# Performance work log

Measured on AMD Instinct MI355X. Metric: run time of the kernel, lower is better.

Reference implementation:

```python
import jax, jax.numpy as jnp
import numpy as np

B, S, HID = 2, 4096, 2048
NH, NKV, HD = 16, 4, 128  # num_heads, num_kv_heads, head_dim
GROUPS = NH // NKV
ROPE_THETA = 10000.0


def _rope_cos_sin(position_ids):
    # position_ids: [B, S] int
    inv_freq = 1.0 / (ROPE_THETA ** (jnp.arange(0, HD, 2, dtype=jnp.float32) / HD))  # [HD/2]
    freqs = position_ids.astype(jnp.float32)[..., None] * inv_freq  # [B, S, HD/2]
    emb = jnp.concatenate([freqs, freqs], axis=-1)  # [B, S, HD]
    return jnp.cos(emb), jnp.sin(emb)


def _rotate_half(x):
    x1, x2 = jnp.split(x, 2, axis=-1)
    return jnp.concatenate([-x2, x1], axis=-1)


def _apply_rope(q, k, cos, sin):
    # q: [B, NH, S, HD], k: [B, NKV, S, HD]; cos/sin: [B, S, HD]
    cos = cos[:, None, :, :]
    sin = sin[:, None, :, :]
    q = q * cos + _rotate_half(q) * sin
    k = k * cos + _rotate_half(k) * sin
    return q, k


def kappa(x):
    return jax.nn.elu(x) + 1.0


def setup_inputs() -> dict:
    key = jax.random.key(0)
    ks = jax.random.split(key, 8)
    sc = 0.02
    hidden_states = jax.random.normal(ks[0], (B, S, HID), dtype=jnp.float32)
    position_ids = jnp.broadcast_to(jnp.arange(S, dtype=jnp.int64)[None, :], (B, S))
    Wq = jax.random.normal(ks[1], (HID, NH * HD), dtype=jnp.float32) * sc
    Wk = jax.random.normal(ks[2], (HID, NKV * HD), dtype=jnp.float32) * sc
    Wv = jax.random.normal(ks[3], (HID, NKV * HD), dtype=jnp.float32) * sc
    Wo = jax.random.normal(ks[4], (HID, HID), dtype=jnp.float32) * sc
    Wphi = jax.random.normal(ks[5], (HID, HID), dtype=jnp.float32) * sc
    bphi = jax.random.normal(ks[6], (HID,), dtype=jnp.float32) * sc
    return {"hidden_states": hidden_states, "position_ids": position_ids,
            "Wq": Wq, "Wk": Wk, "Wv": Wv, "Wo": Wo, "Wphi": Wphi, "bphi": bphi}


def reference(hidden_states, position_ids, Wq, Wk, Wv, Wo, Wphi, bphi):
    b, s, _ = hidden_states.shape
    # projections -> [B, heads, S, HD]
    q = (hidden_states @ Wq).reshape(b, s, NH, HD).transpose(0, 2, 1, 3)
    k = (hidden_states @ Wk).reshape(b, s, NKV, HD).transpose(0, 2, 1, 3)
    v = (hidden_states @ Wv).reshape(b, s, NKV, HD).transpose(0, 2, 1, 3)
    cos, sin = _rope_cos_sin(position_ids)
    q, k = _apply_rope(q, k, cos, sin)
    # GQA expand kv heads
    k = jnp.repeat(k, GROUPS, axis=1)  # [B, NH, S, HD]
    v = jnp.repeat(v, GROUPS, axis=1)
    Qk = kappa(q)
    Kk = kappa(k)
    Qg = Qk.mean(axis=2)  # [B, NH, HD]
    logits = jnp.einsum('bnd,bnsd->bns', Qg, Kk)
    alpha = jax.nn.softmax(logits, axis=-1) * float(s)  # [B, NH, S]
    outer_sum = jnp.einsum('bns,bnsd,bnsf->bndf', alpha, Kk, v)  # [B, NH, HD, HD]
    X_phi = (hidden_states @ Wphi + bphi).reshape(b, s, NH, HD).transpose(0, 2, 1, 3)
    result_attn = jnp.einsum('bnsd,bndf->bnsf', Qk, outer_sum)
    context = (X_phi * result_attn).transpose(0, 2, 1, 3).reshape(b, s, HID)
    return context @ Wo
```

## Files before the change

kernel.cpp:

```cpp
#include <hip/hip_runtime.h>
#include <hip/hip_bf16.h>
#include <math.h>

#define B_    2
#define S_    4096
#define HID_  2048
#define NH_   16
#define NKV_  4
#define HD_   128
#define GROUPS_ (NH_/NKV_)
#define ROPE_THETA_ 10000.0f
#define OSPLIT 8
#define QCH   32

typedef __attribute__((ext_vector_type(8))) short short8;
typedef __attribute__((ext_vector_type(4))) float f32x4;

__device__ inline unsigned short f2bf(float f) {
    __hip_bfloat16 h = __float2bfloat16(f);
    return *(unsigned short*)&h;
}

__device__ inline void gload16(const void* g, void* l) {
    __builtin_amdgcn_global_load_lds((const __attribute__((address_space(1))) void*)g,
                                     (__attribute__((address_space(3))) void*)l, 16, 0, 0);
}

#define BARM() asm volatile("s_barrier" ::: "memory")

__global__ void rope_table_kernel(float* __restrict__ cosT, float* __restrict__ sinT) {
    int s = blockIdx.x;
    int i = threadIdx.x;
    float expo = -2.0f * (float)i / (float)HD_;
    float invf = powf(ROPE_THETA_, expo);
    float f = (float)s * invf;
    cosT[s * 64 + i] = cosf(f);
    sinT[s * 64 + i] = sinf(f);
}

__global__ void cast_bf16_kernel(const float* __restrict__ in,
                                 __hip_bfloat16* __restrict__ out, int n8) {
    int i = blockIdx.x * 256 + threadIdx.x;
    if (i >= n8) return;
    const float4 v0 = *reinterpret_cast<const float4*>(&in[i * 8]);
    const float4 v1 = *reinterpret_cast<const float4*>(&in[i * 8 + 4]);
    union { short8 v; unsigned short u[8]; } o;
    o.u[0] = f2bf(v0.x); o.u[1] = f2bf(v0.y); o.u[2] = f2bf(v0.z); o.u[3] = f2bf(v0.w);
    o.u[4] = f2bf(v1.x); o.u[5] = f2bf(v1.y); o.u[6] = f2bf(v1.z); o.u[7] = f2bf(v1.w);
    *reinterpret_cast<short8*>(&out[i * 8]) = o.v;
}

__global__ __launch_bounds__(256) void transpose_cast_kernel(
        const float* __restrict__ W, __hip_bfloat16* __restrict__ Wt, int K, int N) {
    __shared__ float T[64][65];
    int k0 = blockIdx.y * 64, n0 = blockIdx.x * 64;
    int tid = threadIdx.x;
    int r = tid >> 4, c4 = (tid & 15) * 4;
#pragma unroll
    for (int p = 0; p < 4; ++p) {
        float4 v = *reinterpret_cast<const float4*>(&W[(size_t)(k0 + r + p * 16) * N + n0 + c4]);
        T[r + p * 16][c4 + 0] = v.x;
        T[r + p * 16][c4 + 1] = v.y;
        T[r + p * 16][c4 + 2] = v.z;
        T[r + p * 16][c4 + 3] = v.w;
    }
    __syncthreads();
#pragma unroll
    for (int p = 0; p < 4; ++p) {
        int n = r + p * 16;
        short4 o;
        o.x = (short)f2bf(T[c4 + 0][n]);
        o.y = (short)f2bf(T[c4 + 1][n]);
        o.z = (short)f2bf(T[c4 + 2][n]);
        o.w = (short)f2bf(T[c4 + 3][n]);
        *reinterpret_cast<short4*>(&Wt[(size_t)(n0 + n) * K + k0 + c4]) = o;
    }
}

#define BM 128
#define BN 128
#define BKK 32
__global__ __launch_bounds__(256) void gemm_mfma_kernel(
        const __hip_bfloat16* __restrict__ A, const __hip_bfloat16* __restrict__ Bt,
        float* __restrict__ C, const float* __restrict__ bias, int M, int N, int K) {
    __shared__ __hip_bfloat16 As[BM * BKK];
    __shared__ __hip_bfloat16 Bs[BN * BKK];
    int tid  = threadIdx.x;
    int wid  = tid >> 6, lane = tid & 63;
    int wr   = wid >> 1, wc = wid & 1;
    int bm = blockIdx.y * BM, bn = blockIdx.x * BN;

    f32x4 acc[4][4];
#pragma unroll
    for (int m = 0; m < 4; ++m)
#pragma unroll
        for (int n = 0; n < 4; ++n)
#pragma unroll
            for (int i = 0; i < 4; ++i) acc[m][n][i] = 0.0f;

    int srow = tid >> 2;
    int scol = (tid & 3) * 8;
    const __hip_bfloat16* aS0 = A  + (size_t)(bm + srow)      * K + scol;
    const __hip_bfloat16* aS1 = A  + (size_t)(bm + 64 + srow) * K + scol;
    const __hip_bfloat16* bS0 = Bt + (size_t)(bn + srow)      * K + scol;
    const __hip_bfloat16* bS1 = Bt + (size_t)(bn + 64 + srow) * K + scol;
    __hip_bfloat16* aD0 = &As[wid * 512];
    __hip_bfloat16* aD1 = &As[2048 + wid * 512];
    __hip_bfloat16* bD0 = &Bs[wid * 512];
    __hip_bfloat16* bD1 = &Bs[2048 + wid * 512];

    int lr = lane & 15;
    int kq = (lane >> 4) * 8;

    for (int k0 = 0; k0 < K; k0 += BKK) {
        gload16(aS0 + k0, aD0);
        gload16(aS1 + k0, aD1);
        gload16(bS0 + k0, bD0);
        gload16(bS1 + k0, bD1);
        __syncthreads();

        short8 af[4], bf[4];
#pragma unroll
        for (int m = 0; m < 4; ++m)
            af[m] = *reinterpret_cast<short8*>(&As[(wr * 64 + m * 16 + lr) * BKK + kq]);
#pragma unroll
        for (int n = 0; n < 4; ++n)
            bf[n] = *reinterpret_cast<short8*>(&Bs[(wc * 64 + n * 16 + lr) * BKK + kq]);
#pragma unroll
        for (int m = 0; m < 4; ++m)
#pragma unroll
            for (int n = 0; n < 4; ++n)
                acc[m][n] = __builtin_amdgcn_mfma_f32_16x16x32_bf16(
                    af[m], bf[n], acc[m][n], 0, 0, 0);
        __syncthreads();
    }

    int lq = lane >> 4;
#pragma unroll
    for (int m = 0; m < 4; ++m) {
#pragma unroll
        for (int n = 0; n < 4; ++n) {
            int row = bm + wr * 64 + m * 16 + lq * 4;
            int col = bn + wc * 64 + n * 16 + lr;
            float bv = (bias != nullptr) ? bias[col] : 0.0f;
#pragma unroll
            for (int r = 0; r < 4; ++r)
                C[(size_t)(row + r) * N + col] = acc[m][n][r] + bv;
        }
    }
}

#define TBUFEL 16384

__device__ __forceinline__ void stage_region(const __hip_bfloat16* __restrict__ src,
        int ldK, int row0, int kbase, __hip_bfloat16* dst, int tid) {
#pragma unroll
    for (int g = 0; g < 2; ++g) {
        int P = g * 512 + tid;
        int row = P >> 2, cp = P & 3;
        int cl = cp ^ ((row >> 1) & 3);
        gload16(src + (size_t)(row0 + row) * ldK + kbase + cl * 8, dst + P * 8);
    }
}

__global__ __launch_bounds__(512, 2) void gemm_mfma256_kernel(
        const __hip_bfloat16* __restrict__ A, const __hip_bfloat16* __restrict__ Bt,
        float* __restrict__ C, __hip_bfloat16* __restrict__ Cb,
        const float* __restrict__ bias, int M, int N, int K) {
    __shared__ __hip_bfloat16 lds[4 * TBUFEL];
    int tid = threadIdx.x, lane = tid & 63, wid = tid >> 6;
    int wr = wid >> 2, wc = wid & 3;
    int lr = lane & 15, lc = lane >> 4;
    int c16 = lc ^ ((lr >> 1) & 3);

    int nwg = gridDim.x;
    int orig = blockIdx.x;
    int q = nwg >> 3, r = nwg & 7;
    int xcd = orig & 7, lid = orig >> 3;
    int wg = (xcd < r ? xcd * (q + 1) : r * (q + 1) + (xcd - r) * q) + lid;
    int tiles_n = N >> 8;
    int bm = (wg / tiles_n) << 8, bn = (wg % tiles_n) << 8;

    f32x4 acc[8][4];
#pragma unroll
    for (int m = 0; m < 8; ++m)
#pragma unroll
        for (int n = 0; n < 4; ++n)
#pragma unroll
            for (int i = 0; i < 4; ++i) acc[m][n][i] = 0.0f;

    const int NKT = K >> 5;

    stage_region(A,  K, bm, 0,  lds,                 tid);
    stage_region(Bt, K, bn, 0,  lds + 8192,          tid);
    stage_region(A,  K, bm, 32, lds + TBUFEL,        tid);
    stage_region(Bt, K, bn, 32, lds + TBUFEL + 8192, tid);
    asm volatile("s_waitcnt vmcnt(4)" ::: "memory");
    BARM();

    for (int kt = 0; kt < NKT; ++kt) {
        __hip_bfloat16* buf = lds + (size_t)(kt & 3) * TBUFEL;
        __hip_bfloat16* stg = lds + (size_t)((kt + 2) & 3) * TBUFEL;
        const bool pf = (kt + 2 < NKT);

        if (pf) stage_region(A, K, bm, (kt + 2) << 5, stg, tid);
        short8 a0[4], b0[4];
#pragma unroll
        for (int m = 0; m < 4; ++m)
            a0[m] = *reinterpret_cast<const short8*>(
                &buf[(size_t)(wr * 128 + m * 16 + lr) * 32 + c16 * 8]);
#pragma unroll
        for (int n = 0; n < 4; ++n)
            b0[n] = *reinterpret_cast<const short8*>(
                &buf[8192 + (size_t)(wc * 64 + n * 16 + lr) * 32 + c16 * 8]);
        BARM();
        __builtin_amdgcn_s_setprio(1);
#pragma unroll
        for (int m = 0; m < 4; ++m)
#pragma unroll
            for (int n = 0; n < 4; ++n)
                acc[m][n] = __builtin_amdgcn_mfma_f32_16x16x32_bf16(
                    a0[m], b0[n], acc[m][n], 0, 0, 0);
        __builtin_amdgcn_s_setprio(0);
        BARM();

        if (pf) stage_region(Bt, K, bn, (kt + 2) << 5, stg + 8192, tid);
        short8 a1[4];
#pragma unroll
        for (int m = 0; m < 4; ++m)
            a1[m] = *reinterpret_cast<const short8*>(
                &buf[(size_t)(wr * 128 + 64 + m * 16 + lr) * 32 + c16 * 8]);
        BARM();
        __builtin_amdgcn_s_setprio(1);
#pragma unroll
        for (int m = 0; m < 4; ++m)
#pragma unroll
            for (int n = 0; n < 4; ++n)
                acc[m + 4][n] = __builtin_amdgcn_mfma_f32_16x16x32_bf16(
                    a1[m], b0[n], acc[m + 4][n], 0, 0, 0);
        __builtin_amdgcn_s_setprio(0);
        if (pf) { asm volatile("s_waitcnt vmcnt(4)" ::: "memory"); }
        else    { asm volatile("s_waitcnt vmcnt(0)" ::: "memory"); }
        BARM();
    }

    int lq = lane >> 4;
#pragma unroll
    for (int m = 0; m < 8; ++m) {
#pragma unroll
        for (int n = 0; n < 4; ++n) {
            int row = bm + wr * 128 + m * 16 + lq * 4;
            int col = bn + wc * 64 + n * 16 + lr;
            float bv = (bias != nullptr) ? bias[col] : 0.0f;
            if (Cb != nullptr) {
#pragma unroll
                for (int rr = 0; rr < 4; ++rr)
                    Cb[(size_t)(row + rr) * N + col] = __float2bfloat16(acc[m][n][rr] + bv);
            } else {
#pragma unroll
                for (int rr = 0; rr < 4; ++rr)
                    C[(size_t)(row + rr) * N + col] = acc[m][n][rr] + bv;
            }
        }
    }
}

__global__ void rope_kappa_kernel(float* __restrict__ X,
                                  const float* __restrict__ cosT,
                                  const float* __restrict__ sinT,
                                  int nheads, int rs, int total) {
    int idx = blockIdx.x * blockDim.x + threadIdx.x;
    if (idx >= total) return;
    int d  = idx & 63;
    int t  = idx >> 6;
    int n  = t % nheads;
    int bs = t / nheads;
    int s  = bs % S_;
    size_t base = (size_t)bs * rs + n * HD_;
    float c = cosT[s * 64 + d];
    float sn = sinT[s * 64 + d];
    float x1 = X[base + d];
    float x2 = X[base + d + 64];
    float r1 = x1 * c - x2 * sn;
    float r2 = x2 * c + x1 * sn;
    r1 = (r1 > 0.0f) ? (r1 + 1.0f) : expf(r1);
    r2 = (r2 > 0.0f) ? (r2 + 1.0f) : expf(r2);
    X[base + d] = r1;
    X[base + d + 64] = r2;
}

__global__ __launch_bounds__(128) void qg_partial_kernel(
        const float* __restrict__ Qk, float* __restrict__ QPART) {
    int blk = blockIdx.x;
    int c   = blk % QCH;
    int bn  = blk / QCH;
    int b = bn / NH_, n = bn % NH_;
    int d = threadIdx.x;
    float acc = 0.0f;
    int s0 = c * (S_ / QCH);
    for (int s = s0; s < s0 + S_ / QCH; ++s)
        acc += Qk[((size_t)b * S_ + s) * (NH_ * HD_) + n * HD_ + d];
    QPART[(size_t)(c * (B_ * NH_) + bn) * HD_ + d] = acc;
}

__global__ __launch_bounds__(256) void qg_reduce_kernel(
        const float* __restrict__ QPART, float* __restrict__ QG) {
    int idx = blockIdx.x * 256 + threadIdx.x;
    float acc = 0.0f;
#pragma unroll
    for (int c = 0; c < QCH; ++c)
        acc += QPART[(size_t)c * (B_ * NH_ * HD_) + idx];
    QG[idx] = acc * (1.0f / (float)S_);
}

__global__ __launch_bounds__(256) void logits_kernel(
        const float* __restrict__ KV, const float* __restrict__ QG,
        float* __restrict__ LG) {
    int bk = blockIdx.x;
    int b = bk / NKV_, kn = bk % NKV_;
    int s0 = blockIdx.y * 256;
    int w = threadIdx.x >> 6, lane = threadIdx.x & 63;
    float2 qv[GROUPS_];
#pragma unroll
    for (int g = 0; g < GROUPS_; ++g)
        qv[g] = *reinterpret_cast<const float2*>(
            &QG[(size_t)(b * NH_ + kn * GROUPS_ + g) * HD_ + lane * 2]);
    for (int i = 0; i < 64; ++i) {
        int s = s0 + w * 64 + i;
        float2 kv = *reinterpret_cast<const float2*>(
            &KV[((size_t)b * S_ + s) * 1024 + kn * HD_ + lane * 2]);
        float p[GROUPS_];
#pragma unroll
        for (int g = 0; g < GROUPS_; ++g) p[g] = kv.x * qv[g].x + kv.y * qv[g].y;
#pragma unroll
        for (int off = 32; off > 0; off >>= 1)
#pragma unroll
            for (int g = 0; g < GROUPS_; ++g) p[g] += __shfl_xor(p[g], off);
        if (lane == 0) {
#pragma unroll
            for (int g = 0; g < GROUPS_; ++g)
                LG[(size_t)(b * NH_ + kn * GROUPS_ + g) * S_ + s] = p[g];
        }
    }
}

__global__ __launch_bounds__(256) void softmax_alpha_kernel(float* __restrict__ LG) {
    int bn = blockIdx.x;
    float* row = &LG[(size_t)bn * S_];
    __shared__ float lg[S_];
    __shared__ float red[256];
    int tid = threadIdx.x;
    float lmax = -1e30f;
    for (int s = tid; s < S_; s += 256) {
        float v = row[s];
        lg[s] = v;
        lmax = fmaxf(lmax, v);
    }
    red[tid] = lmax;
    __syncthreads();
    for (int off = 128; off > 0; off >>= 1) {
        if (tid < off) red[tid] = fmaxf(red[tid], red[tid + off]);
        __syncthreads();
    }
    float mx = red[0];
    __syncthreads();
    float lsum = 0.0f;
    for (int s = tid; s < S_; s += 256) {
        float e = expf(lg[s] - mx);
        lg[s] = e;
        lsum += e;
    }
    red[tid] = lsum;
    __syncthreads();
    for (int off = 128; off > 0; off >>= 1) {
        if (tid < off) red[tid] += red[tid + off];
        __syncthreads();
    }
    float inv = (float)S_ / red[0];
    for (int s = tid; s < S_; s += 256)
        row[s] = lg[s] * inv;
}

__global__ __launch_bounds__(256) void kvt_kernel(
        const float* __restrict__ KV, const float* __restrict__ ALPHA,
        __hip_bfloat16* __restrict__ AKT, __hip_bfloat16* __restrict__ VT) {
    int bk = blockIdx.x;
    int b = bk / NKV_, kn = bk % NKV_;
    int s0 = blockIdx.y * 64;
    int isV = blockIdx.z;
    __shared__ float T[64][HD_ + 4];
    __shared__ float alf[GROUPS_][64];
    int tid = threadIdx.x;

    int r = tid >> 2;
    int c0 = (tid & 3) * 32;
    const float* src = KV + ((size_t)(b * S_) + s0 + r) * 1024 + isV * 512 + kn * HD_ + c0;
#pragma unroll
    for (int i = 0; i < 8; ++i)
        *reinterpret_cast<float4*>(&T[r][c0 + i * 4]) =
            *reinterpret_cast<const float4*>(src + i * 4);
    if (!isV) {
        int g = tid >> 6, ss = tid & 63;
        alf[g][ss] = ALPHA[(size_t)(b * NH_ + kn * GROUPS_ + g) * S_ + s0 + ss];
    }
    __syncthreads();

    int d  = tid >> 1;
    int sh = (tid & 1) * 32;
    if (isV) {
        __hip_bfloat16* dst = VT + ((size_t)bk * HD_ + d) * S_ + s0 + sh;
#pragma unroll
        for (int i = 0; i < 8; ++i) {
            short4 o;
            o.x = (short)f2bf(T[sh + i * 4 + 0][d]);
            o.y = (short)f2bf(T[sh + i * 4 + 1][d]);
            o.z = (short)f2bf(T[sh + i * 4 + 2][d]);
            o.w = (short)f2bf(T[sh + i * 4 + 3][d]);
            *reinterpret_cast<short4*>(dst + i * 4) = o;
        }
    } else {
#pragma unroll
        for (int g = 0; g < GROUPS_; ++g) {
            int n = kn * GROUPS_ + g;
            __hip_bfloat16* dst = AKT + ((size_t)(b * NH_ + n) * HD_ + d) * S_ + s0 + sh;
#pragma unroll
            for (int i = 0; i < 8; ++i) {
                short4 o;
                o.x = (short)f2bf(T[sh + i * 4 + 0][d] * alf[g][sh + i * 4 + 0]);
                o.y = (short)f2bf(T[sh + i * 4 + 1][d] * alf[g][sh + i * 4 + 1]);
                o.z = (short)f2bf(T[sh + i * 4 + 2][d] * alf[g][sh + i * 4 + 2]);
                o.w = (short)f2bf(T[sh + i * 4 + 3][d] * alf[g][sh + i * 4 + 3]);
                *reinterpret_cast<short4*>(dst + i * 4) = o;
            }
        }
    }
}

__global__ __launch_bounds__(256) void outer_mfma_kernel(
        const __hip_bfloat16* __restrict__ AKT, const __hip_bfloat16* __restrict__ VT,
        float* __restrict__ OPT) {
    int bn = blockIdx.x;
    int sp = blockIdx.y;
    int b = bn / NH_, n = bn % NH_;
    int kn = n / GROUPS_;
    const __hip_bfloat16* Abase = AKT + (size_t)bn * HD_ * S_ + sp * (S_ / OSPLIT);
    const __hip_bfloat16* Bbase = VT + (size_t)(b * NKV_ + kn) * HD_ * S_ + sp * (S_ / OSPLIT);
    __shared__ __hip_bfloat16 As[128 * 32];
    __shared__ __hip_bfloat16 Bs[128 * 32];
    int tid = threadIdx.x, lane = tid & 63, wid = tid >> 6;
    int wr = wid >> 1, wc = wid & 1;
    int lr = lane & 15, kq = (lane >> 4) * 8;

    f32x4 acc[4][4];
#pragma unroll
    for (int m = 0; m < 4; ++m)
#pragma unroll
        for (int nn = 0; nn < 4; ++nn)
#pragma unroll
            for (int i = 0; i < 4; ++i) acc[m][nn][i] = 0.0f;

    for (int ks = 0; ks < (S_ / OSPLIT) / 32; ++ks) {
        int k0 = ks * 32;
#pragma unroll
        for (int g = 0; g < 2; ++g) {
            int P = g * 256 + tid;
            int row = P >> 2, gr = P & 3;
            gload16(Abase + (size_t)row * S_ + k0 + gr * 8, As + P * 8);
            gload16(Bbase + (size_t)row * S_ + k0 + gr * 8, Bs + P * 8);
        }
        __syncthreads();
        short8 af[4], bf[4];
#pragma unroll
        for (int m = 0; m < 4; ++m)
            af[m] = *reinterpret_cast<short8*>(&As[(wr * 64 + m * 16 + lr) * 32 + kq]);
#pragma unroll
        for (int nn = 0; nn < 4; ++nn)
            bf[nn] = *reinterpret_cast<short8*>(&Bs[(wc * 64 + nn * 16 + lr) * 32 + kq]);
#pragma unroll
        for (int m = 0; m < 4; ++m)
#pragma unroll
            for (int nn = 0; nn < 4; ++nn)
                acc[m][nn] = __builtin_amdgcn_mfma_f32_16x16x32_bf16(
                    af[m], bf[nn], acc[m][nn], 0, 0, 0);
        __syncthreads();
    }

    float* base = OPT + ((size_t)bn * OSPLIT + sp) * (HD_ * HD_);
    int lq = lane >> 4;
#pragma unroll
    for (int m = 0; m < 4; ++m) {
#pragma unroll
        for (int nn = 0; nn < 4; ++nn) {
            int drow = wr * 64 + m * 16 + lq * 4;
            int fcol = wc * 64 + nn * 16 + lr;
            float4 o;
            o.x = acc[m][nn][0]; o.y = acc[m][nn][1];
            o.z = acc[m][nn][2]; o.w = acc[m][nn][3];
            *reinterpret_cast<float4*>(&base[(size_t)fcol * HD_ + drow]) = o;
        }
    }
}

__global__ __launch_bounds__(256) void outer_reduce_tc_kernel(
        const float* __restrict__ OPT, __hip_bfloat16* __restrict__ OUTt) {
    int idx = blockIdx.x * 256 + threadIdx.x;
    int bn = idx >> 11;
    int rem = idx & 2047;
    int f = rem >> 4, g = rem & 15;
    const float* src = OPT + (size_t)bn * OSPLIT * 16384 + f * 128 + g * 8;
    float s[8] = {};
#pragma unroll
    for (int sp = 0; sp < OSPLIT; ++sp) {
        float4 v0 = *reinterpret_cast<const float4*>(src + (size_t)sp * 16384);
        float4 v1 = *reinterpret_cast<const float4*>(src + (size_t)sp * 16384 + 4);
        s[0] += v0.x; s[1] += v0.y; s[2] += v0.z; s[3] += v0.w;
        s[4] += v1.x; s[5] += v1.y; s[6] += v1.z; s[7] += v1.w;
    }
    int gp = g ^ (f & 7);
    union { short8 v; unsigned short u[8]; } o;
#pragma unroll
    for (int j = 0; j < 8; ++j) o.u[j] = f2bf(s[j]);
    *reinterpret_cast<short8*>(&OUTt[(size_t)bn * 16384 + f * 128 + gp * 8]) = o.v;
}

__global__ __launch_bounds__(256) void attn_context_mfma_kernel(
        const float* __restrict__ Qk, const __hip_bfloat16* __restrict__ OUTt,
        const __hip_bfloat16* __restrict__ XPHIb, __hip_bfloat16* __restrict__ CTX) {
    int bn = blockIdx.x;
    int b = bn / NH_, n = bn % NH_;
    int s0 = blockIdx.y * 256;
    __shared__ __hip_bfloat16 Ms[128 * 128];
    int tid = threadIdx.x, lane = tid & 63, wid = tid >> 6;
    int lr = lane & 15, lc = lane >> 4;

#pragma unroll
    for (int g = 0; g < 8; ++g) {
        int P = g * 256 + tid;
        gload16(OUTt + (size_t)bn * 16384 + (size_t)P * 8, Ms + (size_t)P * 8);
    }

    f32x4 acc[4][8];
#pragma unroll
    for (int m = 0; m < 4; ++m)
#pragma unroll
        for (int nn = 0; nn < 8; ++nn)
#pragma unroll
            for (int i = 0; i < 4; ++i) acc[m][nn][i] = 0.0f;

    __syncthreads();

    const float* qbase = Qk + ((size_t)(b * S_) + s0 + wid * 64) * (NH_ * HD_) + n * HD_;
#pragma unroll
    for (int ks = 0; ks < 4; ++ks) {
        int k8 = ks * 32 + lc * 8;
        short8 a[4];
#pragma unroll
        for (int m = 0; m < 4; ++m) {
            const float* qp = qbase + (size_t)(m * 16 + lr) * (NH_ * HD_) + k8;
            float4 q0 = *reinterpret_cast<const float4*>(qp);
            float4 q1 = *reinterpret_cast<const float4*>(qp + 4);
            union { short8 v; unsigned short u[8]; } cv;
            cv.u[0] = f2bf(q0.x); cv.u[1] = f2bf(q0.y); cv.u[2] = f2bf(q0.z); cv.u[3] = f2bf(q0.w);
            cv.u[4] = f2bf(q1.x); cv.u[5] = f2bf(q1.y); cv.u[6] = f2bf(q1.z); cv.u[7] = f2bf(q1.w);
            a[m] = cv.v;
        }
        int gfull = ks * 4 + lc;
        short8 bb[8];
#pragma unroll
        for (int nn = 0; nn < 8; ++nn) {
            int f = nn * 16 + lr;
            int gp = gfull ^ (f & 7);
            bb[nn] = *reinterpret_cast<const short8*>(&Ms[f * 128 + gp * 8]);
        }
#pragma unroll
        for (int m = 0; m < 4; ++m)
#pragma unroll
            for (int nn = 0; nn < 8; ++nn)
                acc[m][nn] = __builtin_amdgcn_mfma_f32_16x16x32_bf16(
                    a[m], bb[nn], acc[m][nn], 0, 0, 0);
    }

#pragma unroll
    for (int m = 0; m < 4; ++m) {
#pragma unroll
        for (int nn = 0; nn < 8; ++nn) {
            int row = s0 + wid * 64 + m * 16 + lc * 4;
            int f = nn * 16 + lr;
            size_t gi = ((size_t)(b * S_) + row) * (NH_ * HD_) + n * HD_ + f;
#pragma unroll
            for (int r = 0; r < 4; ++r) {
                float xp = __bfloat162float(XPHIb[gi + (size_t)r * (NH_ * HD_)]);
                CTX[gi + (size_t)r * (NH_ * HD_)] = __float2bfloat16(acc[m][nn][r] * xp);
            }
        }
    }
}

extern "C" void kernel_launch(void* const* d_in, const int* in_sizes, int n_in,
                              void* d_out, int out_size, void* d_ws, size_t ws_size,
                              hipStream_t stream) {
    (void)in_sizes; (void)n_in; (void)out_size; (void)ws_size;
    const float* X    = (const float*)d_in[0];
    const float* Wq   = (const float*)d_in[2];
    const float* Wk   = (const float*)d_in[3];
    const float* Wv   = (const float*)d_in[4];
    const float* Wo   = (const float*)d_in[5];
    const float* Wphi = (const float*)d_in[6];
    const float* bphi = (const float*)d_in[7];
    float* out = (float*)d_out;

    float* ws = (float*)d_ws;
    const size_t nQ = (size_t)B_ * S_ * NH_ * HD_;
    const size_t nK = (size_t)B_ * S_ * NKV_ * HD_;
    float* Q     = ws;
    float* KV    = Q + nQ;
    float* XPHI  = KV + 2 * nK;
    float* QG    = XPHI + nQ;
    float* ALPHA = QG + (size_t)B_ * NH_ * HD_;
    float* QPART = ALPHA + (size_t)B_ * NH_ * S_;
    float* COST  = QPART + (size_t)QCH * B_ * NH_ * HD_;
    float* SINT  = COST + (size_t)S_ * 64;
    __hip_bfloat16* Xb    = (__hip_bfloat16*)(SINT + (size_t)S_ * 64);
    __hip_bfloat16* Wqt   = Xb + nQ;
    __hip_bfloat16* Wkt   = Wqt + (size_t)HID_ * (NH_ * HD_);
    __hip_bfloat16* Wvt   = Wkt + (size_t)HID_ * (NKV_ * HD_);
    __hip_bfloat16* Wphit = Wvt + (size_t)HID_ * (NKV_ * HD_);
    __hip_bfloat16* Wot   = Wphit + (size_t)HID_ * (NH_ * HD_);
    __hip_bfloat16* OUTt  = Wot + (size_t)HID_ * HID_;
    __hip_bfloat16* VT    = OUTt + (size_t)B_ * NH_ * HD_ * HD_;
    float* OPT = (float*)(VT + nK);
    __hip_bfloat16* AKT   = Xb;
    __hip_bfloat16* XPHIb = (__hip_bfloat16*)XPHI;
    __hip_bfloat16* CTXb  = (__hip_bfloat16*)KV;

    const int M = B_ * S_;

    rope_table_kernel<<<S_, 64, 0, stream>>>(COST, SINT);
    cast_bf16_kernel<<<(int)(nQ / 8 / 256), 256, 0, stream>>>(X, Xb, (int)(nQ / 8));
    transpose_cast_kernel<<<dim3((NH_ * HD_) / 64, HID_ / 64), 256, 0, stream>>>(Wq, Wqt, HID_, NH_ * HD_);
    transpose_cast_kernel<<<dim3((NKV_ * HD_) / 64, HID_ / 64), 256, 0, stream>>>(Wk, Wkt, HID_, NKV_ * HD_);
    transpose_cast_kernel<<<dim3((NKV_ * HD_) / 64, HID_ / 64), 256, 0, stream>>>(Wv, Wvt, HID_, NKV_ * HD_);
    transpose_cast_kernel<<<dim3((NH_ * HD_) / 64, HID_ / 64), 256, 0, stream>>>(Wphi, Wphit, HID_, NH_ * HD_);
    transpose_cast_kernel<<<dim3(HID_ / 64, HID_ / 64), 256, 0, stream>>>(Wo, Wot, HID_, HID_);

    gemm_mfma256_kernel<<<(M / 256) * ((NH_ * HD_) / 256), 512, 0, stream>>>(
        Xb, Wqt, Q, nullptr, nullptr, M, NH_ * HD_, HID_);
    gemm_mfma_kernel<<<dim3(1024 / BN, M / BM), 256, 0, stream>>>(
        Xb, Wkt, KV, nullptr, M, 1024, HID_);
    gemm_mfma256_kernel<<<(M / 256) * ((NH_ * HD_) / 256), 512, 0, stream>>>(
        Xb, Wphit, nullptr, XPHIb, bphi, M, NH_ * HD_, HID_);

    {
        int totalQ = B_ * S_ * NH_ * 64;
        rope_kappa_kernel<<<totalQ / 256, 256, 0, stream>>>(Q, COST, SINT, NH_, NH_ * HD_, totalQ);
        int totalK = B_ * S_ * NKV_ * 64;
        rope_kappa_kernel<<<totalK / 256, 256, 0, stream>>>(KV, COST, SINT, NKV_, 1024, totalK);
    }

    qg_partial_kernel<<<B_ * NH_ * QCH, 128, 0, stream>>>(Q, QPART);
    qg_reduce_kernel<<<(B_ * NH_ * HD_) / 256, 256, 0, stream>>>(QPART, QG);
    logits_kernel<<<dim3(B_ * NKV_, S_ / 256), 256, 0, stream>>>(KV, QG, ALPHA);
    softmax_alpha_kernel<<<B_ * NH_, 256, 0, stream>>>(ALPHA);

    kvt_kernel<<<dim3(B_ * NKV_, S_ / 64, 2), 256, 0, stream>>>(KV, ALPHA, AKT, VT);
    outer_mfma_kernel<<<dim3(B_ * NH_, OSPLIT), 256, 0, stream>>>(AKT, VT, OPT);
    outer_reduce_tc_kernel<<<(B_ * NH_ * HD_ * 16) / 256, 256, 0, stream>>>(OPT, OUTt);

    attn_context_mfma_kernel<<<dim3(B_ * NH_, S_ / 256), 256, 0, stream>>>(
        Q, OUTt, XPHIb, CTXb);

    gemm_mfma256_kernel<<<(M / 256) * (HID_ / 256), 512, 0, stream>>>(
        CTXb, Wot, out, nullptr, nullptr, M, HID_, HID_);
}
```

Baseline: 473.1 us.

## Store Q in bf16, pipeline the 128-tile GEMM, and trim barriers in the 256 GEMM

The Q projection now writes bf16 output. RoPE+kappa, the Qg partial sums and the context kernel all read and write bf16 Q, which halves Q memory traffic and removes the fp32-to-bf16 conversion in the context kernel. The KV GEMM is rewritten with a 4-buffer swizzled LDS prefetch pipeline using global_load_lds and vmcnt waits. In the 256-tile GEMM, both operand stages are issued up front and the intra-iteration barriers are dropped. The trade-offs are a small precision loss in Q before RoPE/kappa and a possible LDS race if the removed barriers were needed.

```diff
diff --git a/kernel.cpp b/kernel.cpp
--- a/kernel.cpp
+++ b/kernel.cpp
@@ -21,6 +21,12 @@
     return *(unsigned short*)&h;
 }
 
+__device__ inline float bf2f(short u) {
+    union { unsigned int i; float f; } v;
+    v.i = ((unsigned int)(unsigned short)u) << 16;
+    return v.f;
+}
+
 __device__ inline void gload16(const void* g, void* l) {
     __builtin_amdgcn_global_load_lds((const __attribute__((address_space(1))) void*)g,
                                      (__attribute__((address_space(3))) void*)l, 16, 0, 0);
@@ -77,81 +83,6 @@
     }
 }
 
-#define BM 128
-#define BN 128
-#define BKK 32
-__global__ __launch_bounds__(256) void gemm_mfma_kernel(
-        const __hip_bfloat16* __restrict__ A, const __hip_bfloat16* __restrict__ Bt,
-        float* __restrict__ C, const float* __restrict__ bias, int M, int N, int K) {
-    __shared__ __hip_bfloat16 As[BM * BKK];
-    __shared__ __hip_bfloat16 Bs[BN * BKK];
-    int tid  = threadIdx.x;
-    int wid  = tid >> 6, lane = tid & 63;
-    int wr   = wid >> 1, wc = wid & 1;
-    int bm = blockIdx.y * BM, bn = blockIdx.x * BN;
-
-    f32x4 acc[4][4];
-#pragma unroll
-    for (int m = 0; m < 4; ++m)
-#pragma unroll
-        for (int n = 0; n < 4; ++n)
-#pragma unroll
-            for (int i = 0; i < 4; ++i) acc[m][n][i] = 0.0f;
-
-    int srow = tid >> 2;
-    int scol = (tid & 3) * 8;
-    const __hip_bfloat16* aS0 = A  + (size_t)(bm + srow)      * K + scol;
-    const __hip_bfloat16* aS1 = A  + (size_t)(bm + 64 + srow) * K + scol;
-    const __hip_bfloat16* bS0 = Bt + (size_t)(bn + srow)      * K + scol;
-    const __hip_bfloat16* bS1 = Bt + (size_t)(bn + 64 + srow) * K + scol;
-    __hip_bfloat16* aD0 = &As[wid * 512];
-    __hip_bfloat16* aD1 = &As[2048 + wid * 512];
-    __hip_bfloat16* bD0 = &Bs[wid * 512];
-    __hip_bfloat16* bD1 = &Bs[2048 + wid * 512];
-
-    int lr = lane & 15;
-    int kq = (lane >> 4) * 8;
-
-    for (int k0 = 0; k0 < K; k0 += BKK) {
-        gload16(aS0 + k0, aD0);
-        gload16(aS1 + k0, aD1);
-        gload16(bS0 + k0, bD0);
-        gload16(bS1 + k0, bD1);
-        __syncthreads();
-
-        short8 af[4], bf[4];
-#pragma unroll
-        for (int m = 0; m < 4; ++m)
-            af[m] = *reinterpret_cast<short8*>(&As[(wr * 64 + m * 16 + lr) * BKK + kq]);
-#pragma unroll
-        for (int n = 0; n < 4; ++n)
-            bf[n] = *reinterpret_cast<short8*>(&Bs[(wc * 64 + n * 16 + lr) * BKK + kq]);
-#pragma unroll
-        for (int m = 0; m < 4; ++m)
-#pragma unroll
-            for (int n = 0; n < 4; ++n)
-                acc[m][n] = __builtin_amdgcn_mfma_f32_16x16x32_bf16(
-                    af[m], bf[n], acc[m][n], 0, 0, 0);
-        __syncthreads();
-    }
-
-    int lq = lane >> 4;
-#pragma unroll
-    for (int m = 0; m < 4; ++m) {
-#pragma unroll
-        for (int n = 0; n < 4; ++n) {
-            int row = bm + wr * 64 + m * 16 + lq * 4;
-            int col = bn + wc * 64 + n * 16 + lr;
-            float bv = (bias != nullptr) ? bias[col] : 0.0f;
-#pragma unroll
-            for (int r = 0; r < 4; ++r)
-                C[(size_t)(row + r) * N + col] = acc[m][n][r] + bv;
-        }
-    }
-}
-
-#define TBUFEL 16384
-
 __device__ __forceinline__ void stage_region(const __hip_bfloat16* __restrict__ src,
         int ldK, int row0, int kbase, __hip_bfloat16* dst, int tid) {
 #pragma unroll
@@ -162,6 +93,95 @@
         gload16(src + (size_t)(row0 + row) * ldK + kbase + cl * 8, dst + P * 8);
     }
 }
+
+__device__ __forceinline__ void stage_region128(const __hip_bfloat16* __restrict__ src,
+        int ldK, int row0, int kbase, __hip_bfloat16* dst, int tid) {
+#pragma unroll
+    for (int g = 0; g < 2; ++g) {
+        int P = g * 256 + tid;
+        int row = P >> 2, cp = P & 3;
+        int cl = cp ^ ((row >> 1) & 3);
+        gload16(src + (size_t)(row0 + row) * ldK + kbase + cl * 8, dst + P * 8);
+    }
+}
+
+#define BM 128
+#define BN 128
+#define T128EL 8192
+__global__ __launch_bounds__(256) void gemm_mfma_kernel(
+        const __hip_bfloat16* __restrict__ A, const __hip_bfloat16* __restrict__ Bt,
+        float* __restrict__ C, const float* __restrict__ bias, int M, int N, int K) {
+    __shared__ __hip_bfloat16 lds[4 * T128EL];
+    int tid  = threadIdx.x;
+    int wid  = tid >> 6, lane = tid & 63;
+    int wr   = wid >> 1, wc = wid & 1;
+    int lr = lane & 15, lc = lane >> 4;
+    int c16 = lc ^ ((lr >> 1) & 3);
+    int bm = blockIdx.y * BM, bn = blockIdx.x * BN;
+
+    f32x4 acc[4][4];
+#pragma unroll
+    for (int m = 0; m < 4; ++m)
+#pragma unroll
+        for (int n = 0; n < 4; ++n)
+#pragma unroll
+            for (int i = 0; i < 4; ++i) acc[m][n][i] = 0.0f;
+
+    const int NKT = K >> 5;
+
+    stage_region128(A,  K, bm, 0,  lds,                 tid);
+    stage_region128(Bt, K, bn, 0,  lds + 4096,          tid);
+    stage_region128(A,  K, bm, 32, lds + T128EL,        tid);
+    stage_region128(Bt, K, bn, 32, lds + T128EL + 4096, tid);
+    asm volatile("s_waitcnt vmcnt(4)" ::: "memory");
+    BARM();
+
+    for (int kt = 0; kt < NKT; ++kt) {
+        __hip_bfloat16* buf = lds + (size_t)(kt & 3) * T128EL;
+        __hip_bfloat16* stg = lds + (size_t)((kt + 2) & 3) * T128EL;
+        const bool pf = (kt + 2 < NKT);
+        if (pf) {
+            stage_region128(A,  K, bm, (kt + 2) << 5, stg,        tid);
+            stage_region128(Bt, K, bn, (kt + 2) << 5, stg + 4096, tid);
+        }
+        short8 af[4], bf[4];
+#pragma unroll
+        for (int m = 0; m < 4; ++m)
+            af[m] = *reinterpret_cast<const short8*>(
+                &buf[(size_t)(wr * 64 + m * 16 + lr) * 32 + c16 * 8]);
+#pragma unroll
+        for (int n = 0; n < 4; ++n)
+            bf[n] = *reinterpret_cast<const short8*>(
+                &buf[4096 + (size_t)(wc * 64 + n * 16 + lr) * 32 + c16 * 8]);
+        __builtin_amdgcn_s_setprio(1);
+#pragma unroll
+        for (int m = 0; m < 4; ++m)
+#pragma unroll
+            for (int n = 0; n < 4; ++n)
+                acc[m][n] = __builtin_amdgcn_mfma_f32_16x16x32_bf16(
+                    af[m], bf[n], acc[m][n], 0, 0, 0);
+        __builtin_amdgcn_s_setprio(0);
+        if (pf) { asm volatile("s_waitcnt vmcnt(4)" ::: "memory"); }
+        else    { asm volatile("s_waitcnt vmcnt(0)" ::: "memory"); }
+        BARM();
+    }
+
+    int lq = lane >> 4;
+#pragma unroll
+    for (int m = 0; m < 4; ++m) {
+#pragma unroll
+        for (int n = 0; n < 4; ++n) {
+            int row = bm + wr * 64 + m * 16 + lq * 4;
+            int col = bn + wc * 64 + n * 16 + lr;
+            float bv = (bias != nullptr) ? bias[col] : 0.0f;
+#pragma unroll
+            for (int r = 0; r < 4; ++r)
+                C[(size_t)(row + r) * N + col] = acc[m][n][r] + bv;
+        }
+    }
+}
+
+#define TBUFEL 16384
 
 __global__ __launch_bounds__(512, 2) void gemm_mfma256_kernel(
         const __hip_bfloat16* __restrict__ A, const __hip_bfloat16* __restrict__ Bt,
@@ -203,17 +223,19 @@
         __hip_bfloat16* stg = lds + (size_t)((kt + 2) & 3) * TBUFEL;
         const bool pf = (kt + 2 < NKT);
 
-        if (pf) stage_region(A, K, bm, (kt + 2) << 5, stg, tid);
-        short8 a0[4], b0[4];
-#pragma unroll
-        for (int m = 0; m < 4; ++m)
-            a0[m] = *reinterpret_cast<const short8*>(
-                &buf[(size_t)(wr * 128 + m * 16 + lr) * 32 + c16 * 8]);
+        if (pf) {
+            stage_region(A,  K, bm, (kt + 2) << 5, stg,        tid);
+            stage_region(Bt, K, bn, (kt + 2) << 5, stg + 8192, tid);
+        }
+        short8 b0[4], a0[4], a1[4];
 #pragma unroll
         for (int n = 0; n < 4; ++n)
             b0[n] = *reinterpret_cast<const short8*>(
                 &buf[8192 + (size_t)(wc * 64 + n * 16 + lr) * 32 + c16 * 8]);
-        BARM();
+#pragma unroll
+        for (int m = 0; m < 4; ++m)
+            a0[m] = *reinterpret_cast<const short8*>(
+                &buf[(size_t)(wr * 128 + m * 16 + lr) * 32 + c16 * 8]);
         __builtin_amdgcn_s_setprio(1);
 #pragma unroll
         for (int m = 0; m < 4; ++m)
@@ -222,15 +244,10 @@
                 acc[m][n] = __builtin_amdgcn_mfma_f32_16x16x32_bf16(
                     a0[m], b0[n], acc[m][n], 0, 0, 0);
         __builtin_amdgcn_s_setprio(0);
-        BARM();
-
-        if (pf) stage_region(Bt, K, bn, (kt + 2) << 5, stg + 8192, tid);
-        short8 a1[4];
 #pragma unroll
         for (int m = 0; m < 4; ++m)
             a1[m] = *reinterpret_cast<const short8*>(
                 &buf[(size_t)(wr * 128 + 64 + m * 16 + lr) * 32 + c16 * 8]);
-        BARM();
         __builtin_amdgcn_s_setprio(1);
 #pragma unroll
         for (int m = 0; m < 4; ++m)
@@ -263,6 +280,42 @@
             }
         }
     }
+}
+
+__global__ void rope_kappa_q_kernel(__hip_bfloat16* __restrict__ Qb,
+                                    const float* __restrict__ cosT,
+                                    const float* __restrict__ sinT, int total) {
+    int idx = blockIdx.x * 256 + threadIdx.x;
+    if (idx >= total) return;
+    int dq = idx & 15;
+    int t  = idx >> 4;
+    int n  = t % NH_;
+    int bs = t / NH_;
+    int s  = bs % S_;
+    size_t base = (size_t)bs * (NH_ * HD_) + n * HD_ + dq * 4;
+    short4 v1 = *reinterpret_cast<short4*>(&Qb[base]);
+    short4 v2 = *reinterpret_cast<short4*>(&Qb[base + 64]);
+    float4 c4 = *reinterpret_cast<const float4*>(&cosT[s * 64 + dq * 4]);
+    float4 s4 = *reinterpret_cast<const float4*>(&sinT[s * 64 + dq * 4]);
+    float x1[4] = {bf2f(v1.x), bf2f(v1.y), bf2f(v1.z), bf2f(v1.w)};
+    float x2[4] = {bf2f(v2.x), bf2f(v2.y), bf2f(v2.z), bf2f(v2.w)};
+    float cc[4] = {c4.x, c4.y, c4.z, c4.w};
+    float ss[4] = {s4.x, s4.y, s4.z, s4.w};
+    short4 o1, o2;
+    short r1s[4], r2s[4];
+#pragma unroll
+    for (int j = 0; j < 4; ++j) {
+        float r1 = x1[j] * cc[j] - x2[j] * ss[j];
+        float r2 = x2[j] * cc[j] + x1[j] * ss[j];
+        r1 = (r1 > 0.0f) ? (r1 + 1.0f) : expf(r1);
+        r2 = (r2 > 0.0f) ? (r2 + 1.0f) : expf(r2);
+        r1s[j] = (short)f2bf(r1);
+        r2s[j] = (short)f2bf(r2);
+    }
+    o1.x = r1s[0]; o1.y = r1s[1]; o1.z = r1s[2]; o1.w = r1s[3];
+    o2.x = r2s[0]; o2.y = r2s[1]; o2.z = r2s[2]; o2.w = r2s[3];
+    *reinterpret_cast<short4*>(&Qb[base])      = o1;
+    *reinterpret_cast<short4*>(&Qb[base + 64]) = o2;
 }
 
 __global__ void rope_kappa_kernel(float* __restrict__ X,
@@ -289,18 +342,33 @@
     X[base + d + 64] = r2;
 }
 
-__global__ __launch_bounds__(128) void qg_partial_kernel(
-        const float* __restrict__ Qk, float* __restrict__ QPART) {
+__global__ __launch_bounds__(256) void qg_partial_kernel(
+        const __hip_bfloat16* __restrict__ Qb, float* __restrict__ QPART) {
     int blk = blockIdx.x;
     int c   = blk % QCH;
     int bn  = blk / QCH;
     int b = bn / NH_, n = bn % NH_;
-    int d = threadIdx.x;
-    float acc = 0.0f;
+    int t = threadIdx.x;
+    int d8 = (t & 15) * 8;
+    int sg = t >> 4;
+    float acc[8] = {};
     int s0 = c * (S_ / QCH);
-    for (int s = s0; s < s0 + S_ / QCH; ++s)
-        acc += Qk[((size_t)b * S_ + s) * (NH_ * HD_) + n * HD_ + d];
-    QPART[(size_t)(c * (B_ * NH_) + bn) * HD_ + d] = acc;
+    for (int s = s0 + sg; s < s0 + S_ / QCH; s += 16) {
+        short8 v = *reinterpret_cast<const short8*>(
+            &Qb[((size_t)b * S_ + s) * (NH_ * HD_) + n * HD_ + d8]);
+#pragma unroll
+        for (int j = 0; j < 8; ++j) acc[j] += bf2f(v[j]);
+    }
+    __shared__ float red[16][128];
+#pragma unroll
+    for (int j = 0; j < 8; ++j) red[sg][d8 + j] = acc[j];
+    __syncthreads();
+    if (t < 128) {
+        float s = 0.0f;
+#pragma unroll
+        for (int g = 0; g < 16; ++g) s += red[g][t];
+        QPART[(size_t)(c * (B_ * NH_) + bn) * HD_ + t] = s;
+    }
 }
 
 __global__ __launch_bounds__(256) void qg_reduce_kernel(
@@ -524,7 +592,7 @@
 }
 
 __global__ __launch_bounds__(256) void attn_context_mfma_kernel(
-        const float* __restrict__ Qk, const __hip_bfloat16* __restrict__ OUTt,
+        const __hip_bfloat16* __restrict__ Qb, const __hip_bfloat16* __restrict__ OUTt,
         const __hip_bfloat16* __restrict__ XPHIb, __hip_bfloat16* __restrict__ CTX) {
     int bn = blockIdx.x;
     int b = bn / NH_, n = bn % NH_;
@@ -549,21 +617,16 @@
 
     __syncthreads();
 
-    const float* qbase = Qk + ((size_t)(b * S_) + s0 + wid * 64) * (NH_ * HD_) + n * HD_;
+    const __hip_bfloat16* qbase =
+        Qb + ((size_t)(b * S_) + s0 + wid * 64) * (NH_ * HD_) + n * HD_;
 #pragma unroll
     for (int ks = 0; ks < 4; ++ks) {
         int k8 = ks * 32 + lc * 8;
         short8 a[4];
 #pragma unroll
-        for (int m = 0; m < 4; ++m) {
-            const float* qp = qbase + (size_t)(m * 16 + lr) * (NH_ * HD_) + k8;
-            float4 q0 = *reinterpret_cast<const float4*>(qp);
-            float4 q1 = *reinterpret_cast<const float4*>(qp + 4);
-            union { short8 v; unsigned short u[8]; } cv;
-            cv.u[0] = f2bf(q0.x); cv.u[1] = f2bf(q0.y); cv.u[2] = f2bf(q0.z); cv.u[3] = f2bf(q0.w);
-            cv.u[4] = f2bf(q1.x); cv.u[5] = f2bf(q1.y); cv.u[6] = f2bf(q1.z); cv.u[7] = f2bf(q1.w);
-            a[m] = cv.v;
-        }
+        for (int m = 0; m < 4; ++m)
+            a[m] = *reinterpret_cast<const short8*>(
+                qbase + (size_t)(m * 16 + lr) * (NH_ * HD_) + k8);
         int gfull = ks * 4 + lc;
         short8 bb[8];
 #pragma unroll
@@ -629,6 +692,7 @@
     __hip_bfloat16* OUTt  = Wot + (size_t)HID_ * HID_;
     __hip_bfloat16* VT    = OUTt + (size_t)B_ * NH_ * HD_ * HD_;
     float* OPT = (float*)(VT + nK);
+    __hip_bfloat16* Qb    = (__hip_bfloat16*)Q;
     __hip_bfloat16* AKT   = Xb;
     __hip_bfloat16* XPHIb = (__hip_bfloat16*)XPHI;
     __hip_bfloat16* CTXb  = (__hip_bfloat16*)KV;
@@ -644,20 +708,20 @@
     transpose_cast_kernel<<<dim3(HID_ / 64, HID_ / 64), 256, 0, stream>>>(Wo, Wot, HID_, HID_);
 
     gemm_mfma256_kernel<<<(M / 256) * ((NH_ * HD_) / 256), 512, 0, stream>>>(
-        Xb, Wqt, Q, nullptr, nullptr, M, NH_ * HD_, HID_);
+        Xb, Wqt, nullptr, Qb, nullptr, M, NH_ * HD_, HID_);
     gemm_mfma_kernel<<<dim3(1024 / BN, M / BM), 256, 0, stream>>>(
         Xb, Wkt, KV, nullptr, M, 1024, HID_);
     gemm_mfma256_kernel<<<(M / 256) * ((NH_ * HD_) / 256), 512, 0, stream>>>(
         Xb, Wphit, nullptr, XPHIb, bphi, M, NH_ * HD_, HID_);
 
     {
-        int totalQ = B_ * S_ * NH_ * 64;
-        rope_kappa_kernel<<<totalQ / 256, 256, 0, stream>>>(Q, COST, SINT, NH_, NH_ * HD_, totalQ);
+        int totalQ = B_ * S_ * NH_ * 16;
+        rope_kappa_q_kernel<<<totalQ / 256, 256, 0, stream>>>(Qb, COST, SINT, totalQ);
         int totalK = B_ * S_ * NKV_ * 64;
         rope_kappa_kernel<<<totalK / 256, 256, 0, stream>>>(KV, COST, SINT, NKV_, 1024, totalK);
     }
 
-    qg_partial_kernel<<<B_ * NH_ * QCH, 128, 0, stream>>>(Q, QPART);
+    qg_partial_kernel<<<B_ * NH_ * QCH, 256, 0, stream>>>(Qb, QPART);
     qg_reduce_kernel<<<(B_ * NH_ * HD_) / 256, 256, 0, stream>>>(QPART, QG);
     logits_kernel<<<dim3(B_ * NKV_, S_ / 256), 256, 0, stream>>>(KV, QG, ALPHA);
     softmax_alpha_kernel<<<B_ * NH_, 256, 0, stream>>>(ALPHA);
@@ -667,7 +731,7 @@
     outer_reduce_tc_kernel<<<(B_ * NH_ * HD_ * 16) / 256, 256, 0, stream>>>(OPT, OUTt);
 
     attn_context_mfma_kernel<<<dim3(B_ * NH_, S_ / 256), 256, 0, stream>>>(
-        Q, OUTt, XPHIb, CTXb);
+        Qb, OUTt, XPHIb, CTXb);
 
     gemm_mfma256_kernel<<<(M / 256) * (HID_ / 256), 512, 0, stream>>>(
         CTXb, Wot, out, nullptr, nullptr, M, HID_, HID_);
```

Result: faster. 440.1 us (-7.0%).
